# Kernel optimization log

Hardware: AMD Instinct MI355X
Metric: run time of the kernel (lower is better)

## Reference

```python
import jax, jax.numpy as jnp
import numpy as np

N_NODES = 50000
N_EDGES = 400000
N_GRAPHS = 512
NF = 64      # node_features
EF = 32      # edge_features (RBF bins)
AIF = 92     # atom_input_features
FC = 128     # fc_features
L = 3        # conv layers
EPS = 1e-5   # BatchNorm eps


def _bn(x, gamma, beta):
    # BatchNorm1d, training-mode statistics over the batch (edge/node) dim
    m = x.mean(0)
    v = x.var(0)  # biased variance, matches torch normalization
    return (x - m) * jax.lax.rsqrt(v + EPS) * gamma + beta


def _rbf(d):
    # RBFExpansion(vmin=0, vmax=8, bins=EF): gamma = 1/mean(diff(centers))
    centers = jnp.linspace(0.0, 8.0, EF)
    gamma = 1.0 / (centers[1] - centers[0])
    return jnp.exp(-gamma * (d[:, None] - centers) ** 2)  # [E, EF]


def setup_inputs() -> dict:
    key = jax.random.key(0)
    ks = jax.random.split(key, 12)
    s = 0.05
    IN = 2 * NF + EF
    return {
        "atom_features": jax.random.normal(ks[0], (N_NODES, AIF), dtype=jnp.float32),
        "bondlength": jax.random.uniform(ks[1], (N_EDGES,), dtype=jnp.float32) * 8.0,
        "src": jax.random.randint(ks[2], (N_EDGES,), 0, N_NODES),
        "dst": jax.random.randint(ks[3], (N_EDGES,), 0, N_NODES),
        "graph_ids": jnp.sort(jax.random.randint(ks[4], (N_NODES,), 0, N_GRAPHS)),
        "W_emb": jax.random.normal(ks[5], (AIF, NF), dtype=jnp.float32) * s,
        "b_emb": jnp.zeros((NF,), jnp.float32),
        "Wi": jax.random.normal(ks[6], (L, IN, NF), dtype=jnp.float32) * s,
        "bi": jnp.zeros((L, NF), jnp.float32),
        "gi": jnp.ones((L, NF), jnp.float32),
        "bti": jnp.zeros((L, NF), jnp.float32),
        "Wu": jax.random.normal(ks[7], (L, IN, NF), dtype=jnp.float32) * s,
        "bu": jnp.zeros((L, NF), jnp.float32),
        "gu": jnp.ones((L, NF), jnp.float32),
        "btu": jnp.zeros((L, NF), jnp.float32),
        "g_bn": jnp.ones((L, NF), jnp.float32),
        "b_bn": jnp.zeros((L, NF), jnp.float32),
        "W_fc": jax.random.normal(ks[8], (NF, FC), dtype=jnp.float32) * s,
        "b_fc": jnp.zeros((FC,), jnp.float32),
        "W_out": jax.random.normal(ks[9], (FC, 1), dtype=jnp.float32) * s,
        "b_out": jnp.zeros((1,), jnp.float32),
    }


def reference(atom_features, bondlength, src, dst, graph_ids,
              W_emb, b_emb, Wi, bi, gi, bti, Wu, bu, gu, btu,
              g_bn, b_bn, W_fc, b_fc, W_out, b_out):
    e = _rbf(bondlength)                       # [E, EF]
    h = atom_features @ W_emb + b_emb          # [N, NF]
    for l in range(L):
        # gather + concat: [E, 2*NF + EF]
        z = jnp.concatenate([h[src], h[dst], e], axis=1)
        gate = jax.nn.sigmoid(_bn(z @ Wi[l] + bi[l], gi[l], bti[l]))
        upd = jax.nn.softplus(_bn(z @ Wu[l] + bu[l], gu[l], btu[l]))
        msg = gate * upd                       # [E, NF]
        agg = jax.ops.segment_sum(msg, dst, num_segments=N_NODES)
        h = jax.nn.softplus(h + _bn(agg, g_bn[l], b_bn[l]))
    # AvgPooling over nodes per graph
    counts = jax.ops.segment_sum(jnp.ones((N_NODES, 1), h.dtype), graph_ids,
                                 num_segments=N_GRAPHS)
    pooled = jax.ops.segment_sum(h, graph_ids, num_segments=N_GRAPHS)
    pooled = pooled / jnp.maximum(counts, 1.0)  # [G, NF]
    f = jax.nn.softplus(pooled)
    f = jax.nn.softplus(f @ W_fc + b_fc)
    f = jax.nn.softplus(f)
    out = f @ W_out + b_out                    # [G, 1]
    return jnp.squeeze(out)                    # [G]
```

## Files before the change

### kernel.cpp

```cpp
#include <hip/hip_runtime.h>
#include <math.h>

#define N_NODES 50000
#define N_EDGES 400000
#define N_GRAPHS 512
#define TBL 2048
#define EPSBN 1e-5f

__device__ __forceinline__ float softplusf(float x) {
  return fmaxf(x, 0.0f) + log1pf(expf(-fabsf(x)));
}
__device__ __forceinline__ float sigmoidf(float x) {
  return 1.0f / (1.0f + expf(-x));
}
__device__ __forceinline__ void fma4(float4& acc, float s, const float4& w) {
  acc.x = fmaf(s, w.x, acc.x);
  acc.y = fmaf(s, w.y, acc.y);
  acc.z = fmaf(s, w.z, acc.z);
  acc.w = fmaf(s, w.w, acc.w);
}

__global__ void k_emb(const float* __restrict__ atom,
                      const float* __restrict__ Wemb,
                      const float* __restrict__ bemb,
                      float* __restrict__ h) {
  __shared__ float sW[92 * 64];
  __shared__ float sA[32 * 92];
  const int tid = threadIdx.x;
  for (int i = tid; i < 92 * 64; i += 256) sW[i] = Wemb[i];

  const int t0 = blockIdx.x * 32;
  const int nt = min(32, N_NODES - t0);
  {
    const float* srcp = atom + (size_t)t0 * 92;
    const int tot = nt * 92;
    for (int i = tid; i < tot; i += 256) sA[i] = srcp[i];
  }
  __syncthreads();

  const int col = tid & 63;
  const int ng = tid >> 6;
  const float bb = bemb[col];
  float acc[8];
#pragma unroll
  for (int i = 0; i < 8; ++i) acc[i] = bb;

  for (int kc = 0; kc < 92; kc += 4) {
    const float w0 = sW[(kc + 0) * 64 + col];
    const float w1 = sW[(kc + 1) * 64 + col];
    const float w2 = sW[(kc + 2) * 64 + col];
    const float w3 = sW[(kc + 3) * 64 + col];
#pragma unroll
    for (int i = 0; i < 8; ++i) {
      const float4 a = *(const float4*)&sA[(ng * 8 + i) * 92 + kc];
      acc[i] = fmaf(a.x, w0, acc[i]);
      acc[i] = fmaf(a.y, w1, acc[i]);
      acc[i] = fmaf(a.z, w2, acc[i]);
      acc[i] = fmaf(a.w, w3, acc[i]);
    }
  }
#pragma unroll
  for (int i = 0; i < 8; ++i) {
    const int n = t0 + ng * 8 + i;
    if (n < N_NODES) h[(size_t)n * 64 + col] = acc[i];
  }
}

__global__ void k_pq(const float* __restrict__ h,
                     const float* __restrict__ Wi_l,
                     const float* __restrict__ Wu_l,
                     float* __restrict__ PA,
                     float* __restrict__ PB) {
  __shared__ float sWA[64 * 128];
  __shared__ float sWB[64 * 128];
  __shared__ float sH[32 * 64];
  const int tid = threadIdx.x;

  for (int i = tid; i < 64 * 64; i += 256) {
    const int k = i >> 6, c = i & 63;
    sWA[k * 128 + c]      = Wi_l[k * 64 + c];
    sWA[k * 128 + 64 + c] = Wu_l[k * 64 + c];
    sWB[k * 128 + c]      = Wi_l[(64 + k) * 64 + c];
    sWB[k * 128 + 64 + c] = Wu_l[(64 + k) * 64 + c];
  }
  const int t0 = blockIdx.x * 32;
  const int nt = min(32, N_NODES - t0);
  {
    const float4* srcp = (const float4*)(h + (size_t)t0 * 64);
    const int tot4 = nt * 16;
    float4* dstp = (float4*)sH;
    for (int i = tid; i < tot4; i += 256) dstp[i] = srcp[i];
  }
  __syncthreads();

  const int wave = tid >> 6, lane = tid & 63;
  const float* wcol = (lane < 32) ? (sWA + 4 * lane) : (sWB + 4 * (lane - 32));
  const int jj = (lane < 32) ? 4 * lane : 4 * (lane - 32);
  float* OUTb = (lane < 32) ? PA : PB;

  float4 acc[8];
#pragma unroll
  for (int i = 0; i < 8; ++i) acc[i] = make_float4(0.f, 0.f, 0.f, 0.f);

  for (int kc = 0; kc < 64; kc += 4) {
    const float4 w0 = *(const float4*)(wcol + (kc + 0) * 128);
    const float4 w1 = *(const float4*)(wcol + (kc + 1) * 128);
    const float4 w2 = *(const float4*)(wcol + (kc + 2) * 128);
    const float4 w3 = *(const float4*)(wcol + (kc + 3) * 128);
#pragma unroll
    for (int i = 0; i < 8; ++i) {
      const float4 a = *(const float4*)&sH[(wave * 8 + i) * 64 + kc];
      fma4(acc[i], a.x, w0);
      fma4(acc[i], a.y, w1);
      fma4(acc[i], a.z, w2);
      fma4(acc[i], a.w, w3);
    }
  }
#pragma unroll
  for (int i = 0; i < 8; ++i) {
    const int n = t0 + wave * 8 + i;
    if (n < N_NODES) *(float4*)&OUTb[(size_t)n * 128 + jj] = acc[i];
  }
}

__global__ void k_tbl(const float* __restrict__ Wi_l,
                      const float* __restrict__ Wu_l,
                      float* __restrict__ tbl) {
  const int wave = threadIdx.x >> 6, lane = threadIdx.x & 63;
  const int t = blockIdx.x * (blockDim.x >> 6) + wave;
  if (t >= TBL) return;
  const float d = 8.0f * (float)t / (float)(TBL - 1);
  float gi_ = 0.f, gu_ = 0.f;
#pragma unroll
  for (int k = 0; k < 32; ++k) {
    const float c = 8.0f * (float)k / 31.0f;
    const float dd = d - c;
    const float r = expf(-3.875f * dd * dd);
    gi_ = fmaf(r, Wi_l[(128 + k) * 64 + lane], gi_);
    gu_ = fmaf(r, Wu_l[(128 + k) * 64 + lane], gu_);
  }
  tbl[(size_t)t * 128 + lane] = gi_;
  tbl[(size_t)t * 128 + 64 + lane] = gu_;
}

__global__ void k_deg(const int* __restrict__ dst, int* __restrict__ deg) {
  const int stride = blockDim.x * gridDim.x;
  for (int e = blockIdx.x * blockDim.x + threadIdx.x; e < N_EDGES; e += stride)
    atomicAdd(&deg[dst[e]], 1);
}

__global__ void k_scan(const int* __restrict__ deg, int* __restrict__ offs,
                       int* __restrict__ cursor) {
  __shared__ int part[1024];
  const int t = threadIdx.x;
  const int CHUNK = (N_NODES + 1023) / 1024;
  const int base = t * CHUNK;
  int s = 0;
  for (int i = 0; i < CHUNK; ++i) {
    const int idx = base + i;
    if (idx < N_NODES) s += deg[idx];
  }
  part[t] = s;
  __syncthreads();
  for (int off = 1; off < 1024; off <<= 1) {
    int v = (t >= off) ? part[t - off] : 0;
    __syncthreads();
    part[t] += v;
    __syncthreads();
  }
  int run = (t > 0) ? part[t - 1] : 0;
  for (int i = 0; i < CHUNK; ++i) {
    const int idx = base + i;
    if (idx < N_NODES) {
      offs[idx] = run;
      cursor[idx] = run;
      run += deg[idx];
    }
  }
  if (t == 1023) offs[N_NODES] = run;
}

__global__ void k_scatter(const int* __restrict__ src, const int* __restrict__ dst,
                          const float* __restrict__ bond,
                          int* __restrict__ cursor,
                          int* __restrict__ csr_src, float* __restrict__ csr_d) {
  const int stride = blockDim.x * gridDim.x;
  for (int e = blockIdx.x * blockDim.x + threadIdx.x; e < N_EDGES; e += stride) {
    const int p = atomicAdd(&cursor[dst[e]], 1);
    csr_src[p] = src[e];
    csr_d[p] = bond[e];
  }
}

__device__ __forceinline__ void csr_edge(int k, int lane,
                                         const int* __restrict__ csr_src,
                                         const float* __restrict__ csr_d,
                                         const float* __restrict__ PA,
                                         const float* __restrict__ tbl,
                                         float& pg, float& pu) {
  const int s = csr_src[k];
  const float d = csr_d[k];
  float f = d * ((float)(TBL - 1) / 8.0f);
  f = fminf(fmaxf(f, 0.0f), (float)(TBL - 1));
  int i0 = (int)f;
  if (i0 > TBL - 2) i0 = TBL - 2;
  const float fr = f - (float)i0;
  const float* ta = tbl + (size_t)i0 * 128 + lane;
  const float rg = fmaf(fr, ta[128] - ta[0], ta[0]);
  const float ru = fmaf(fr, ta[192] - ta[64], ta[64]);
  const float* pa = PA + (size_t)s * 128 + lane;
  pg = pa[0] + rg;
  pu = pa[64] + ru;
}

__global__ void k_stats_csr(const int* __restrict__ offs,
                            const int* __restrict__ csr_src,
                            const float* __restrict__ csr_d,
                            const float* __restrict__ PA,
                            const float* __restrict__ PB,
                            const float* __restrict__ tbl,
                            float* __restrict__ stats) {
  const int wave = threadIdx.x >> 6, lane = threadIdx.x & 63;
  const int wpb = blockDim.x >> 6;
  const int nw = wpb * gridDim.x;
  float sg = 0.f, qg = 0.f, su = 0.f, qu = 0.f;
  for (int n = blockIdx.x * wpb + wave; n < N_NODES; n += nw) {
    const float pbg = PB[(size_t)n * 128 + lane];
    const float pbu = PB[(size_t)n * 128 + 64 + lane];
    const int k0 = offs[n], k1 = offs[n + 1];
    for (int k = k0; k < k1; ++k) {
      float pg, pu;
      csr_edge(k, lane, csr_src, csr_d, PA, tbl, pg, pu);
      const float yg = pg + pbg;
      const float yu = pu + pbu;
      sg += yg; qg = fmaf(yg, yg, qg);
      su += yu; qu = fmaf(yu, yu, qu);
    }
  }
  __shared__ float red[4][4][64];
  red[0][wave][lane] = sg;
  red[1][wave][lane] = qg;
  red[2][wave][lane] = su;
  red[3][wave][lane] = qu;
  __syncthreads();
  const float v = red[wave][0][lane] + red[wave][1][lane] +
                  red[wave][2][lane] + red[wave][3][lane];
  atomicAdd(&stats[wave * 64 + lane], v);
}

__global__ void k_fin_gu(const float* __restrict__ stats,
                         const float* __restrict__ gi_l, const float* __restrict__ bti_l,
                         const float* __restrict__ gu_l, const float* __restrict__ btu_l,
                         float* __restrict__ coefs) {
  const int j = threadIdx.x;
  const float invE = 1.0f / (float)N_EDGES;
  float m = stats[j] * invE;
  float v = stats[64 + j] * invE - m * m;
  float a = gi_l[j] * rsqrtf(v + EPSBN);
  coefs[j] = a;
  coefs[64 + j] = fmaf(-m, a, bti_l[j]);
  m = stats[128 + j] * invE;
  v = stats[192 + j] * invE - m * m;
  a = gu_l[j] * rsqrtf(v + EPSBN);
  coefs[128 + j] = a;
  coefs[192 + j] = fmaf(-m, a, btu_l[j]);
}

__global__ void k_apply_csr(const int* __restrict__ offs,
                            const int* __restrict__ csr_src,
                            const float* __restrict__ csr_d,
                            const float* __restrict__ PA,
                            const float* __restrict__ PB,
                            const float* __restrict__ tbl,
                            const float* __restrict__ coefs,
                            float* __restrict__ agg,
                            float* __restrict__ stats) {
  const int wave = threadIdx.x >> 6, lane = threadIdx.x & 63;
  const int wpb = blockDim.x >> 6;
  const int nw = wpb * gridDim.x;
  const float ag = coefs[lane], bg = coefs[64 + lane];
  const float au = coefs[128 + lane], bu = coefs[192 + lane];
  float s2 = 0.f, q2 = 0.f;
  for (int n = blockIdx.x * wpb + wave; n < N_NODES; n += nw) {
    const float pbg = PB[(size_t)n * 128 + lane];
    const float pbu = PB[(size_t)n * 128 + 64 + lane];
    const int k0 = offs[n], k1 = offs[n + 1];
    float acc = 0.f;
    for (int k = k0; k < k1; ++k) {
      float pg, pu;
      csr_edge(k, lane, csr_src, csr_d, PA, tbl, pg, pu);
      const float gate = sigmoidf(fmaf(ag, pg + pbg, bg));
      const float upd = softplusf(fmaf(au, pu + pbu, bu));
      acc = fmaf(gate, upd, acc);
    }
    agg[(size_t)n * 64 + lane] = acc;
    s2 += acc;
    q2 = fmaf(acc, acc, q2);
  }
  __shared__ float red[2][4][64];
  red[0][wave][lane] = s2;
  red[1][wave][lane] = q2;
  __syncthreads();
  if (wave < 2) {
    const float v = red[wave][0][lane] + red[wave][1][lane] +
                    red[wave][2][lane] + red[wave][3][lane];
    atomicAdd(&stats[256 + wave * 64 + lane], v);
  }
}

__global__ void k_fin_agg(const float* __restrict__ stats,
                          const float* __restrict__ gbn_l, const float* __restrict__ bbn_l,
                          float* __restrict__ coefs) {
  const int j = threadIdx.x;
  const float invN = 1.0f / (float)N_NODES;
  const float m = stats[256 + j] * invN;
  const float v = stats[320 + j] * invN - m * m;
  const float a = gbn_l[j] * rsqrtf(v + EPSBN);
  coefs[256 + j] = a;
  coefs[320 + j] = fmaf(-m, a, bbn_l[j]);
}

__global__ void k_hupd(float* __restrict__ h, const float* __restrict__ agg,
                       const float* __restrict__ coefs) {
  const int stride = blockDim.x * gridDim.x;
  for (int i = blockIdx.x * blockDim.x + threadIdx.x; i < N_NODES * 64; i += stride) {
    const int j = i & 63;
    const float x = h[i] + fmaf(coefs[256 + j], agg[i], coefs[320 + j]);
    h[i] = softplusf(x);
  }
}

__global__ void k_pool(const float* __restrict__ h, const int* __restrict__ gid,
                       float* __restrict__ pooled, float* __restrict__ counts) {
  const int lane = threadIdx.x & 63;
  const int wg = blockIdx.x * (blockDim.x >> 6) + (threadIdx.x >> 6);
  const int nwaves = (blockDim.x >> 6) * gridDim.x;
  const int chunk = (N_NODES + nwaves - 1) / nwaves;
  const int n0 = wg * chunk;
  if (n0 >= N_NODES) return;
  const int n1 = min(n0 + chunk, N_NODES);
  int cur = gid[n0];
  float acc = 0.f, cnt = 0.f;
  for (int n = n0; n < n1; ++n) {
    const int g = gid[n];
    if (g != cur) {
      atomicAdd(&pooled[(size_t)cur * 64 + lane], acc);
      if (lane == 0) atomicAdd(&counts[cur], cnt);
      cur = g; acc = 0.f; cnt = 0.f;
    }
    acc += h[(size_t)n * 64 + lane];
    cnt += 1.0f;
  }
  atomicAdd(&pooled[(size_t)cur * 64 + lane], acc);
  if (lane == 0) atomicAdd(&counts[cur], cnt);
}

__global__ void k_final(const float* __restrict__ pooled, const float* __restrict__ counts,
                        const float* __restrict__ Wfc, const float* __restrict__ bfc,
                        const float* __restrict__ Wout, const float* __restrict__ bout,
                        float* __restrict__ out) {
  __shared__ float f1[64];
  __shared__ float red[128];
  const int g = blockIdx.x, t = threadIdx.x;
  if (t < 64) {
    const float c = fmaxf(counts[g], 1.0f);
    f1[t] = softplusf(pooled[(size_t)g * 64 + t] / c);
  }
  __syncthreads();
  float acc = bfc[t];
#pragma unroll
  for (int k = 0; k < 64; ++k) acc = fmaf(f1[k], Wfc[k * 128 + t], acc);
  red[t] = softplusf(softplusf(acc)) * Wout[t];
  __syncthreads();
  for (int s2 = 64; s2 > 0; s2 >>= 1) {
    if (t < s2) red[t] += red[t + s2];
    __syncthreads();
  }
  if (t == 0) out[g] = red[0] + bout[0];
}

extern "C" void kernel_launch(void* const* d_in, const int* in_sizes, int n_in,
                              void* d_out, int out_size, void* d_ws, size_t ws_size,
                              hipStream_t stream) {
  const float* atom = (const float*)d_in[0];
  const float* bond = (const float*)d_in[1];
  const int* src = (const int*)d_in[2];
  const int* dst = (const int*)d_in[3];
  const int* gid = (const int*)d_in[4];
  const float* Wemb = (const float*)d_in[5];
  const float* bemb = (const float*)d_in[6];
  const float* Wi = (const float*)d_in[7];
  const float* gi = (const float*)d_in[9];
  const float* bti = (const float*)d_in[10];
  const float* Wu = (const float*)d_in[11];
  const float* gub = (const float*)d_in[13];
  const float* btu = (const float*)d_in[14];
  const float* gbn = (const float*)d_in[15];
  const float* bbn = (const float*)d_in[16];
  const float* Wfc = (const float*)d_in[17];
  const float* bfc = (const float*)d_in[18];
  const float* Wout = (const float*)d_in[19];
  const float* bout = (const float*)d_in[20];

  float* h = (float*)d_ws;
  float* PA = h + (size_t)N_NODES * 64;
  float* PB = PA + (size_t)N_NODES * 128;
  float* agg = PB + (size_t)N_NODES * 128;
  float* tbl = agg + (size_t)N_NODES * 64;
  float* stats = tbl + (size_t)TBL * 128;
  float* coefs = stats + 384;
  float* pooled = coefs + 384;
  float* counts = pooled + (size_t)N_GRAPHS * 64;
  int* deg = (int*)(counts + N_GRAPHS);
  int* offs = deg + N_NODES;
  int* cursor = offs + N_NODES + 1;
  int* csr_src = cursor + N_NODES;
  float* csr_d = (float*)(csr_src + N_EDGES);

  const int ntiles = (N_NODES + 31) / 32;

  (void)hipMemsetAsync(deg, 0, (size_t)N_NODES * sizeof(int), stream);
  k_emb<<<ntiles, 256, 0, stream>>>(atom, Wemb, bemb, h);
  k_deg<<<512, 256, 0, stream>>>(dst, deg);
  k_scan<<<1, 1024, 0, stream>>>(deg, offs, cursor);
  k_scatter<<<512, 256, 0, stream>>>(src, dst, bond, cursor, csr_src, csr_d);

  for (int l = 0; l < 3; ++l) {
    const float* Wi_l = Wi + (size_t)l * 160 * 64;
    const float* Wu_l = Wu + (size_t)l * 160 * 64;
    (void)hipMemsetAsync(stats, 0, 384 * sizeof(float), stream);
    k_pq<<<ntiles, 256, 0, stream>>>(h, Wi_l, Wu_l, PA, PB);
    k_tbl<<<TBL / 4, 256, 0, stream>>>(Wi_l, Wu_l, tbl);
    k_stats_csr<<<2048, 256, 0, stream>>>(offs, csr_src, csr_d, PA, PB, tbl, stats);
    k_fin_gu<<<1, 64, 0, stream>>>(stats, gi + l * 64, bti + l * 64,
                                   gub + l * 64, btu + l * 64, coefs);
    k_apply_csr<<<2048, 256, 0, stream>>>(offs, csr_src, csr_d, PA, PB, tbl,
                                          coefs, agg, stats);
    k_fin_agg<<<1, 64, 0, stream>>>(stats, gbn + l * 64, bbn + l * 64, coefs);
    k_hupd<<<1024, 256, 0, stream>>>(h, agg, coefs);
  }
  (void)hipMemsetAsync(pooled, 0, (size_t)(N_GRAPHS * 64 + N_GRAPHS) * sizeof(float), stream);
  k_pool<<<512, 256, 0, stream>>>(h, gid, pooled, counts);
  k_final<<<N_GRAPHS, 128, 0, stream>>>(pooled, counts, Wfc, bfc, Wout, bout,
                                        (float*)d_out);
}
```

Measured before the change: 1.792 ms.

## Fuse node update into next-layer projection and pooling, replace memsets, unroll edge loops

Removes the standalone h-update kernel. The softplus residual update of h is now applied while the next layer's projection kernel loads its node tile, and for the last layer inside the pooling kernel. The stats, deg and pooled memsets are replaced by zeroing inside kernels that already run: a small k_fence kernel and block 0 of k_pq. The per-node CSR edge loops in the stats and apply kernels are unrolled by two so more independent gathers are in flight. This saves a full read/write pass over h per layer and several launches, but adds per-element transcendental work and a scalar, non-vectorised load path in k_pq.

```diff
diff --git a/kernel.cpp b/kernel.cpp
--- a/kernel.cpp
+++ b/kernel.cpp
@@ -18,6 +18,17 @@
   acc.y = fmaf(s, w.y, acc.y);
   acc.z = fmaf(s, w.z, acc.z);
   acc.w = fmaf(s, w.w, acc.w);
+}
+
+__global__ void k_fence(int* __restrict__ deg, float* __restrict__ pooled,
+                        float* __restrict__ counts) {
+  const int stride = blockDim.x * gridDim.x;
+  for (int i = blockIdx.x * blockDim.x + threadIdx.x; i < N_NODES; i += stride)
+    deg[i] = 0;
+  for (int i = blockIdx.x * blockDim.x + threadIdx.x; i < N_GRAPHS * 64; i += stride)
+    pooled[i] = 0.f;
+  for (int i = blockIdx.x * blockDim.x + threadIdx.x; i < N_GRAPHS; i += stride)
+    counts[i] = 0.f;
 }
 
 __global__ void k_emb(const float* __restrict__ atom,
@@ -66,15 +77,23 @@
   }
 }
 
-__global__ void k_pq(const float* __restrict__ h,
+__global__ void k_pq(float* __restrict__ h,
+                     const float* __restrict__ agg,
+                     const float* __restrict__ coefs,
+                     const int do_upd,
                      const float* __restrict__ Wi_l,
                      const float* __restrict__ Wu_l,
                      float* __restrict__ PA,
-                     float* __restrict__ PB) {
+                     float* __restrict__ PB,
+                     float* __restrict__ stats) {
   __shared__ float sWA[64 * 128];
   __shared__ float sWB[64 * 128];
   __shared__ float sH[32 * 64];
   const int tid = threadIdx.x;
+
+  if (blockIdx.x == 0) {
+    for (int i = tid; i < 384; i += 256) stats[i] = 0.f;
+  }
 
   for (int i = tid; i < 64 * 64; i += 256) {
     const int k = i >> 6, c = i & 63;
@@ -86,10 +105,19 @@
   const int t0 = blockIdx.x * 32;
   const int nt = min(32, N_NODES - t0);
   {
-    const float4* srcp = (const float4*)(h + (size_t)t0 * 64);
-    const int tot4 = nt * 16;
-    float4* dstp = (float4*)sH;
-    for (int i = tid; i < tot4; i += 256) dstp[i] = srcp[i];
+    float* hp = h + (size_t)t0 * 64;
+    const int tot = nt * 64;
+    if (do_upd) {
+      const float* ap = agg + (size_t)t0 * 64;
+      for (int i = tid; i < tot; i += 256) {
+        const int j = i & 63;
+        const float v = softplusf(hp[i] + fmaf(coefs[256 + j], ap[i], coefs[320 + j]));
+        hp[i] = v;
+        sH[i] = v;
+      }
+    } else {
+      for (int i = tid; i < tot; i += 256) sH[i] = hp[i];
+    }
   }
   __syncthreads();
 
@@ -228,11 +256,22 @@
     const float pbg = PB[(size_t)n * 128 + lane];
     const float pbu = PB[(size_t)n * 128 + 64 + lane];
     const int k0 = offs[n], k1 = offs[n + 1];
-    for (int k = k0; k < k1; ++k) {
+    int k = k0;
+    for (; k + 1 < k1; k += 2) {
+      float pg0, pu0, pg1, pu1;
+      csr_edge(k, lane, csr_src, csr_d, PA, tbl, pg0, pu0);
+      csr_edge(k + 1, lane, csr_src, csr_d, PA, tbl, pg1, pu1);
+      const float yg0 = pg0 + pbg, yu0 = pu0 + pbu;
+      const float yg1 = pg1 + pbg, yu1 = pu1 + pbu;
+      sg += yg0 + yg1;
+      qg = fmaf(yg0, yg0, qg); qg = fmaf(yg1, yg1, qg);
+      su += yu0 + yu1;
+      qu = fmaf(yu0, yu0, qu); qu = fmaf(yu1, yu1, qu);
+    }
+    if (k < k1) {
       float pg, pu;
       csr_edge(k, lane, csr_src, csr_d, PA, tbl, pg, pu);
-      const float yg = pg + pbg;
-      const float yu = pu + pbu;
+      const float yg = pg + pbg, yu = pu + pbu;
       sg += yg; qg = fmaf(yg, yg, qg);
       su += yu; qu = fmaf(yu, yu, qu);
     }
@@ -286,7 +325,19 @@
     const float pbu = PB[(size_t)n * 128 + 64 + lane];
     const int k0 = offs[n], k1 = offs[n + 1];
     float acc = 0.f;
-    for (int k = k0; k < k1; ++k) {
+    int k = k0;
+    for (; k + 1 < k1; k += 2) {
+      float pg0, pu0, pg1, pu1;
+      csr_edge(k, lane, csr_src, csr_d, PA, tbl, pg0, pu0);
+      csr_edge(k + 1, lane, csr_src, csr_d, PA, tbl, pg1, pu1);
+      const float g0 = sigmoidf(fmaf(ag, pg0 + pbg, bg));
+      const float u0 = softplusf(fmaf(au, pu0 + pbu, bu));
+      const float g1 = sigmoidf(fmaf(ag, pg1 + pbg, bg));
+      const float u1 = softplusf(fmaf(au, pu1 + pbu, bu));
+      acc = fmaf(g0, u0, acc);
+      acc = fmaf(g1, u1, acc);
+    }
+    if (k < k1) {
       float pg, pu;
       csr_edge(k, lane, csr_src, csr_d, PA, tbl, pg, pu);
       const float gate = sigmoidf(fmaf(ag, pg + pbg, bg));
@@ -320,17 +371,9 @@
   coefs[320 + j] = fmaf(-m, a, bbn_l[j]);
 }
 
-__global__ void k_hupd(float* __restrict__ h, const float* __restrict__ agg,
-                       const float* __restrict__ coefs) {
-  const int stride = blockDim.x * gridDim.x;
-  for (int i = blockIdx.x * blockDim.x + threadIdx.x; i < N_NODES * 64; i += stride) {
-    const int j = i & 63;
-    const float x = h[i] + fmaf(coefs[256 + j], agg[i], coefs[320 + j]);
-    h[i] = softplusf(x);
-  }
-}
-
-__global__ void k_pool(const float* __restrict__ h, const int* __restrict__ gid,
+__global__ void k_pool(const float* __restrict__ h, const float* __restrict__ agg,
+                       const float* __restrict__ coefs,
+                       const int* __restrict__ gid,
                        float* __restrict__ pooled, float* __restrict__ counts) {
   const int lane = threadIdx.x & 63;
   const int wg = blockIdx.x * (blockDim.x >> 6) + (threadIdx.x >> 6);
@@ -339,6 +382,7 @@
   const int n0 = wg * chunk;
   if (n0 >= N_NODES) return;
   const int n1 = min(n0 + chunk, N_NODES);
+  const float a = coefs[256 + lane], b = coefs[320 + lane];
   int cur = gid[n0];
   float acc = 0.f, cnt = 0.f;
   for (int n = n0; n < n1; ++n) {
@@ -348,7 +392,8 @@
       if (lane == 0) atomicAdd(&counts[cur], cnt);
       cur = g; acc = 0.f; cnt = 0.f;
     }
-    acc += h[(size_t)n * 64 + lane];
+    const size_t idx = (size_t)n * 64 + lane;
+    acc += softplusf(h[idx] + fmaf(a, agg[idx], b));
     cnt += 1.0f;
   }
   atomicAdd(&pooled[(size_t)cur * 64 + lane], acc);
@@ -419,7 +464,7 @@
 
   const int ntiles = (N_NODES + 31) / 32;
 
-  (void)hipMemsetAsync(deg, 0, (size_t)N_NODES * sizeof(int), stream);
+  k_fence<<<104, 256, 0, stream>>>(deg, pooled, counts);
   k_emb<<<ntiles, 256, 0, stream>>>(atom, Wemb, bemb, h);
   k_deg<<<512, 256, 0, stream>>>(dst, deg);
   k_scan<<<1, 1024, 0, stream>>>(deg, offs, cursor);
@@ -428,8 +473,8 @@
   for (int l = 0; l < 3; ++l) {
     const float* Wi_l = Wi + (size_t)l * 160 * 64;
     const float* Wu_l = Wu + (size_t)l * 160 * 64;
-    (void)hipMemsetAsync(stats, 0, 384 * sizeof(float), stream);
-    k_pq<<<ntiles, 256, 0, stream>>>(h, Wi_l, Wu_l, PA, PB);
+    k_pq<<<ntiles, 256, 0, stream>>>(h, agg, coefs, (l > 0) ? 1 : 0,
+                                     Wi_l, Wu_l, PA, PB, stats);
     k_tbl<<<TBL / 4, 256, 0, stream>>>(Wi_l, Wu_l, tbl);
     k_stats_csr<<<2048, 256, 0, stream>>>(offs, csr_src, csr_d, PA, PB, tbl, stats);
     k_fin_gu<<<1, 64, 0, stream>>>(stats, gi + l * 64, bti + l * 64,
@@ -437,10 +482,8 @@
     k_apply_csr<<<2048, 256, 0, stream>>>(offs, csr_src, csr_d, PA, PB, tbl,
                                           coefs, agg, stats);
     k_fin_agg<<<1, 64, 0, stream>>>(stats, gbn + l * 64, bbn + l * 64, coefs);
-    k_hupd<<<1024, 256, 0, stream>>>(h, agg, coefs);
-  }
-  (void)hipMemsetAsync(pooled, 0, (size_t)(N_GRAPHS * 64 + N_GRAPHS) * sizeof(float), stream);
-  k_pool<<<512, 256, 0, stream>>>(h, gid, pooled, counts);
+  }
+  k_pool<<<512, 256, 0, stream>>>(h, agg, coefs, gid, pooled, counts);
   k_final<<<N_GRAPHS, 128, 0, stream>>>(pooled, counts, Wfc, bfc, Wout, bout,
                                         (float*)d_out);
 }
```

Result: no change. 1.806 ms (+0.8%).
